# Optimization experiments

Hardware: AMD Instinct MI355X
Metric: run time of the kernel (lower is better)

The kernel has to match this reference:

```python
import jax, jax.numpy as jnp
import numpy as np

N_ENT, E, M, STEPS, B, H, C = 500000, 128, 8, 3, 4096, 256, 16

def setup_inputs() -> dict:
    key = jax.random.key(0)
    ks = jax.random.split(key, 13)
    s = 0.05
    return {
        "entity_ids": jax.random.randint(ks[0], (B, STEPS + 1), 0, N_ENT),
        "module_ids": jax.random.randint(ks[1], (B, STEPS), 0, M),
        "embedding": jax.random.normal(ks[2], (N_ENT, E), jnp.float32),
        "W_in": jax.random.normal(ks[3], (M, E, E), jnp.float32) * s,
        "b_in": jax.random.normal(ks[4], (M, E), jnp.float32) * s,
        "W_bias": jax.random.normal(ks[5], (M, E, E), jnp.float32) * s,
        "b_bias": jax.random.normal(ks[6], (M, E), jnp.float32) * s,
        "W_f": jax.random.normal(ks[7], (M, 2 * E, E), jnp.float32) * s,
        "b_f": jax.random.normal(ks[8], (M, E), jnp.float32) * s,
        "W1": jax.random.normal(ks[9], (E, H), jnp.float32) * s,
        "b1": jax.random.normal(ks[10], (H,), jnp.float32) * s,
        "W2": jax.random.normal(ks[11], (H, C), jnp.float32) * s,
        "b2": jax.random.normal(ks[12], (C,), jnp.float32) * s,
    }

def reference(entity_ids, module_ids, embedding, W_in, b_in, W_bias, b_bias,
              W_f, b_f, W1, b1, W2, b2):
    # x: [B, E] embedding of each path's start entity
    x = embedding[entity_ids[:, 0]]

    def step(x, inputs):
        mid, eid = inputs                      # [B], [B]
        bias = embedding[eid]                  # [B, E]
        h_in = jax.nn.relu(jnp.einsum('be,beo->bo', x, W_in[mid]) + b_in[mid])
        h_bi = jax.nn.relu(jnp.einsum('be,beo->bo', bias, W_bias[mid]) + b_bias[mid])
        h = jnp.concatenate([h_in, h_bi], axis=1)  # [B, 2E]
        x_new = jnp.tanh(jnp.einsum('bf,bfo->bo', h, W_f[mid]) + b_f[mid])
        return x_new, None

    xs = (module_ids.T, entity_ids[:, 1:].T)   # [STEPS, B] each
    x, _ = jax.lax.scan(step, x, xs)

    # classifier: Linear -> ReLU -> Linear
    h = jax.nn.relu(x @ W1 + b1)
    return h @ W2 + b2
```

## Files before the change

### kernel.cpp

```cpp
#include <hip/hip_runtime.h>

#define BB      4096
#define EE      128
#define MM      8
#define NSTEPS  3
#define HH      256
#define CC      16

#define TS      16
#define FB      1024

#define NFRAGBLK 1096

#define NSEG    8
#define GRIDN   256
#define PREP_GRID (NFRAGBLK + NSTEPS*NSEG + 8)

typedef __attribute__((ext_vector_type(8))) short  bf16x8;
typedef __attribute__((ext_vector_type(4))) float  f32x4;

__device__ __forceinline__ unsigned short bf16_rn(float v) {
    unsigned u = __float_as_uint(v);
    return (unsigned short)((u + 0x7FFFu + ((u >> 16) & 1u)) >> 16);
}
__device__ __forceinline__ float bf16_f(unsigned short h) {
    return __uint_as_float(((unsigned)h) << 16);
}
__device__ __forceinline__ void split8(const float* v, bf16x8& hi, bf16x8& lo) {
    #pragma unroll
    for (int i = 0; i < 8; i++) {
        unsigned short h = bf16_rn(v[i]);
        hi[i] = (short)h;
        lo[i] = (short)bf16_rn(v[i] - bf16_f(h));
    }
}
__device__ __forceinline__ void split1(float v, unsigned short& h, unsigned short& l) {
    h = bf16_rn(v);
    l = bf16_rn(v - bf16_f(h));
}
#define MFMA(a,b,c) __builtin_amdgcn_mfma_f32_16x16x32_bf16((a),(b),(c),0,0,0)
__device__ __forceinline__ f32x4 mfma3(bf16x8 ah, bf16x8 al, bf16x8 bh, bf16x8 bl, f32x4 c) {
    c = MFMA(ah, bh, c);
    c = MFMA(ah, bl, c);
    c = MFMA(al, bh, c);
    return c;
}

__global__ __launch_bounds__(512) void prep_kernel(
    const int*   __restrict__ module_ids,
    const float* __restrict__ W_in, const float* __restrict__ W_bias,
    const float* __restrict__ W_f,  const float* __restrict__ W1,
    const float* __restrict__ W2,
    unsigned short* __restrict__ wf,
    int* __restrict__ wcnt, int* __restrict__ perm, int* __restrict__ fl)
{
    const int vb = blockIdx.x, tid = threadIdx.x;
    __shared__ int wc8[8][MM];

    if (vb < NFRAGBLK) {
        unsigned short* dhi = wf + (size_t)vb * FB;
        unsigned short* dlo = dhi + 512;
        const int el = tid;
        const int ln = el >> 3, j = el & 7;
        const int krel = ((ln >> 4) << 3) + j;
        const int nrel = ln & 15;
        float v;
        if (vb < 512) {
            const int bb = vb & 255;
            const int kc = bb & 3, nt = (bb >> 2) & 7, m = bb >> 5;
            const float* src = (vb < 256 ? W_in : W_bias) + (size_t)m * EE * EE;
            v = src[(size_t)(kc*32 + krel) * EE + nt*16 + nrel];
        } else if (vb < 1024) {
            const int bb = vb - 512;
            const int kc = bb & 7, nt = (bb >> 3) & 7, m = bb >> 6;
            v = W_f[(size_t)m * 2*EE*EE + (size_t)(kc*32 + krel) * EE + nt*16 + nrel];
        } else if (vb < 1088) {
            const int bb = vb - 1024;
            const int kc = bb & 3, nt = bb >> 2;
            v = W1[(size_t)(kc*32 + krel) * HH + nt*16 + nrel];
        } else {
            const int kc = vb - 1088;
            v = W2[(size_t)(kc*32 + krel) * CC + nrel];
        }
        split1(v, dhi[el], dlo[el]);
    } else if (vb < NFRAGBLK + NSTEPS*NSEG) {
        const int u = vb - NFRAGBLK;
        const int t = u >> 3, seg = u & 7;
        const int lane = tid & 63, wave = tid >> 6;
        const int s = seg*512 + tid;
        const int m = module_ids[s*NSTEPS + t];
        unsigned long long mybal = 0ull, lanebal = 0ull;
        #pragma unroll
        for (int k = 0; k < MM; k++) {
            const unsigned long long bk = __ballot(m == k);
            if (m == k)    mybal   = bk;
            if (lane == k) lanebal = bk;
        }
        if (lane < MM) wc8[wave][lane] = __popcll(lanebal);
        __syncthreads();
        int base = 0;
        #pragma unroll
        for (int w = 0; w < 8; w++) if (w < wave) base += wc8[w][m];
        const unsigned long long below = (1ull << lane) - 1ull;
        const int rank = __popcll(mybal & below);
        perm[(((t*MM + m)*NSEG) + seg)*512 + base + rank] = s;
        if (tid < MM) {
            int sum = 0;
            #pragma unroll
            for (int w = 0; w < 8; w++) sum += wc8[w][tid];
            wcnt[((t*MM + tid)*NSEG) + seg] = sum;
        }
    } else {
        const int u = vb - NFRAGBLK - NSTEPS*NSEG;
        fl[u*512 + tid] = 0;
    }
}

__global__ __launch_bounds__(512, 2) void steps_kernel(
    const int*   __restrict__ entity_ids,
    const float* __restrict__ embedding,
    const float* __restrict__ b_in, const float* __restrict__ b_bias,
    const float* __restrict__ b_f,
    const float* __restrict__ b1v, const float* __restrict__ b2,
    const unsigned short* __restrict__ wf,
    const int* __restrict__ wcnt, const int* __restrict__ perm,
    unsigned short* __restrict__ xsh, unsigned short* __restrict__ xsl,
    int* __restrict__ fl, float* __restrict__ out)
{
    const int bx = blockIdx.x, tid = threadIdx.x;
    const int lane = tid & 63, wave = tid >> 6;
    const int row16 = lane & 15, quad = lane >> 4;

    __shared__ __align__(16) unsigned short hfh[8][512];
    __shared__ __align__(16) unsigned short hfl[8][512];
    __shared__ int   sids[TS];
    __shared__ float red[8][TS][CC];

    for (int t = 0; t < NSTEPS; t++) {
        int tot[MM];
        #pragma unroll
        for (int k = 0; k < MM; k++) {
            int s = 0;
            #pragma unroll
            for (int j = 0; j < NSEG; j++) s += wcnt[(t*MM + k)*NSEG + j];
            tot[k] = s;
        }
        int NB = 0;
        #pragma unroll
        for (int k = 0; k < MM; k++) NB += (tot[k] + TS - 1) >> 4;

        for (int pass = 0; pass < 2; pass++) {
            const int vb = bx + pass*GRIDN;
            if (vb >= NB) break;

            int m = -1, pref = 0, cm = 0, acc = 0;
            #pragma unroll
            for (int k = 0; k < MM; k++) {
                const int nbk = (tot[k] + TS - 1) >> 4;
                if (m < 0 && vb < acc + nbk) { m = k; pref = acc; cm = tot[k]; }
                acc += nbk;
            }
            const int chunk = vb - pref;

            __syncthreads();
            if (tid < TS) {
                const int sl = chunk*TS + tid;
                int sv = -1;
                if (sl < cm) {
                    int j = 0, r = sl;
                    while (true) {
                        const int c = wcnt[(t*MM + m)*NSEG + j];
                        if (r < c) break;
                        r -= c; j++;
                    }
                    sv = perm[((t*MM + m)*NSEG + j)*512 + r];
                }
                sids[tid] = sv;
            }
            __syncthreads();

            const int sA  = sids[row16];
            const int sAc = sA < 0 ? 0 : sA;

            bf16x8 xh[4], xl[4], eh[4], el_[4];
            const int eidb = entity_ids[sAc*(NSTEPS+1) + t + 1];
            const float* srcb = embedding + (size_t)eidb*EE;

            if (t == 0) {
                const int eid0 = entity_ids[sAc*(NSTEPS+1)];
                const float* src0 = embedding + (size_t)eid0*EE;
                #pragma unroll
                for (int kc = 0; kc < 4; kc++) {
                    const int off = kc*32 + quad*8;
                    float vv[8], bb[8];
                    *(float4*)(vv)     = *(const float4*)(src0 + off);
                    *(float4*)(vv + 4) = *(const float4*)(src0 + off + 4);
                    *(float4*)(bb)     = *(const float4*)(srcb + off);
                    *(float4*)(bb + 4) = *(const float4*)(srcb + off + 4);
                    split8(vv, xh[kc], xl[kc]);
                    split8(bb, eh[kc], el_[kc]);
                }
            } else {
                float bb[4][8];
                #pragma unroll
                for (int kc = 0; kc < 4; kc++) {
                    const int off = kc*32 + quad*8;
                    *(float4*)(bb[kc])     = *(const float4*)(srcb + off);
                    *(float4*)(bb[kc] + 4) = *(const float4*)(srcb + off + 4);
                }
                if (tid < TS && sids[tid] >= 0) {
                    int* f = &fl[sids[tid]];
                    while (__hip_atomic_load(f, __ATOMIC_RELAXED, __HIP_MEMORY_SCOPE_AGENT) < t)
                        __builtin_amdgcn_s_sleep(2);
                    (void)__hip_atomic_load(f, __ATOMIC_ACQUIRE, __HIP_MEMORY_SCOPE_AGENT);
                }
                __syncthreads();

                const unsigned short* xhp = xsh + (size_t)sAc*EE;
                const unsigned short* xlp = xsl + (size_t)sAc*EE;
                #pragma unroll
                for (int kc = 0; kc < 4; kc++) {
                    const int off = kc*32 + quad*8;
                    xh[kc] = *(const bf16x8*)(xhp + off);
                    xl[kc] = *(const bf16x8*)(xlp + off);
                    split8(bb[kc], eh[kc], el_[kc]);
                }
            }

            f32x4 aci = {0.f,0.f,0.f,0.f}, acb = {0.f,0.f,0.f,0.f};
            #pragma unroll
            for (int kc = 0; kc < 4; kc++) {
                const unsigned short* bI  = wf + (size_t)((m*8 + wave)*4 + kc)*FB;
                const unsigned short* bBp = wf + (size_t)(256 + (m*8 + wave)*4 + kc)*FB;
                const bf16x8 wih = *(const bf16x8*)(bI + lane*8);
                const bf16x8 wil = *(const bf16x8*)(bI + 512 + lane*8);
                const bf16x8 wbh = *(const bf16x8*)(bBp + lane*8);
                const bf16x8 wbl = *(const bf16x8*)(bBp + 512 + lane*8);
                aci = mfma3(xh[kc], xl[kc], wih, wil, aci);
                acb = mfma3(eh[kc], el_[kc], wbh, wbl, acb);
            }

            {
                const int col = wave*16 + row16;
                const float bin = b_in [m*EE + col];
                const float bbi = b_bias[m*EE + col];
                #pragma unroll
                for (int r = 0; r < 4; r++) {
                    const int row = quad*4 + r;
                    {
                        const float v = fmaxf(aci[r] + bin, 0.f);
                        const int k = col, kc = k >> 5;
                        const int idx = (row + 16*((k >> 3) & 3))*8 + (k & 7);
                        split1(v, hfh[kc][idx], hfl[kc][idx]);
                    }
                    {
                        const float v = fmaxf(acb[r] + bbi, 0.f);
                        const int k = EE + col, kc = k >> 5;
                        const int idx = (row + 16*((k >> 3) & 3))*8 + (k & 7);
                        split1(v, hfh[kc][idx], hfl[kc][idx]);
                    }
                }
            }
            __syncthreads();

            f32x4 acf = {0.f,0.f,0.f,0.f};
            #pragma unroll
            for (int kc = 0; kc < 8; kc++) {
                const bf16x8 ah = *(const bf16x8*)(&hfh[kc][lane*8]);
                const bf16x8 al = *(const bf16x8*)(&hfl[kc][lane*8]);
                const unsigned short* bF = wf + (size_t)(512 + (m*8 + wave)*8 + kc)*FB;
                const bf16x8 wfh = *(const bf16x8*)(bF + lane*8);
                const bf16x8 wfl = *(const bf16x8*)(bF + 512 + lane*8);
                acf = mfma3(ah, al, wfh, wfl, acf);
            }

            const int col = wave*16 + row16;
            const float bfv = b_f[m*EE + col];
            float xv[4];
            #pragma unroll
            for (int r = 0; r < 4; r++) xv[r] = tanhf(acf[r] + bfv);

            if (t < NSTEPS-1) {
                #pragma unroll
                for (int r = 0; r < 4; r++) {
                    const int s = sids[quad*4 + r];
                    if (s >= 0) {
                        unsigned short h, l;
                        split1(xv[r], h, l);
                        xsh[(size_t)s*EE + col] = h;
                        xsl[(size_t)s*EE + col] = l;
                    }
                }
                __syncthreads();
                if (tid < TS && sids[tid] >= 0)
                    __hip_atomic_store(&fl[sids[tid]], t+1,
                                       __ATOMIC_RELEASE, __HIP_MEMORY_SCOPE_AGENT);
            } else {
                __syncthreads();
                #pragma unroll
                for (int r = 0; r < 4; r++) {
                    const int row = quad*4 + r;
                    const int k = col, kc = k >> 5;
                    const int idx = (row + 16*((k >> 3) & 3))*8 + (k & 7);
                    split1(xv[r], hfh[kc][idx], hfl[kc][idx]);
                }
                __syncthreads();

                f32x4 a1[2] = {{0.f,0.f,0.f,0.f},{0.f,0.f,0.f,0.f}};
                #pragma unroll
                for (int i = 0; i < 2; i++) {
                    const int nt = wave + 8*i;
                    #pragma unroll
                    for (int kc = 0; kc < 4; kc++) {
                        const unsigned short* bW = wf + (size_t)(1024 + nt*4 + kc)*FB;
                        const bf16x8 wh = *(const bf16x8*)(bW + lane*8);
                        const bf16x8 wl = *(const bf16x8*)(bW + 512 + lane*8);
                        const bf16x8 ah = *(const bf16x8*)(&hfh[kc][lane*8]);
                        const bf16x8 al = *(const bf16x8*)(&hfl[kc][lane*8]);
                        a1[i] = mfma3(ah, al, wh, wl, a1[i]);
                    }
                }
                __syncthreads();
                #pragma unroll
                for (int i = 0; i < 2; i++) {
                    const int c2 = (wave + 8*i)*16 + row16;
                    const float b = b1v[c2];
                    #pragma unroll
                    for (int r = 0; r < 4; r++) {
                        const int row = quad*4 + r;
                        const float v = fmaxf(a1[i][r] + b, 0.f);
                        const int kc = c2 >> 5;
                        const int idx = (row + 16*((c2 >> 3) & 3))*8 + (c2 & 7);
                        split1(v, hfh[kc][idx], hfl[kc][idx]);
                    }
                }
                __syncthreads();

                f32x4 a2 = {0.f,0.f,0.f,0.f};
                {
                    const int kc = wave;
                    const bf16x8 ah = *(const bf16x8*)(&hfh[kc][lane*8]);
                    const bf16x8 al = *(const bf16x8*)(&hfl[kc][lane*8]);
                    const unsigned short* bW = wf + (size_t)(1088 + kc)*FB;
                    const bf16x8 wh = *(const bf16x8*)(bW + lane*8);
                    const bf16x8 wl = *(const bf16x8*)(bW + 512 + lane*8);
                    a2 = mfma3(ah, al, wh, wl, a2);
                }
                #pragma unroll
                for (int r = 0; r < 4; r++) red[wave][quad*4 + r][row16] = a2[r];
                __syncthreads();

                if (tid < TS*CC) {
                    const int sr = sids[tid >> 4];
                    if (sr >= 0) {
                        const int c = tid & 15;
                        float v = b2[c];
                        #pragma unroll
                        for (int w = 0; w < 8; w++) v += red[w][tid >> 4][c];
                        out[(size_t)sr*CC + c] = v;
                    }
                }
            }
        }
    }
}

extern "C" void kernel_launch(void* const* d_in, const int* in_sizes, int n_in,
                              void* d_out, int out_size, void* d_ws, size_t ws_size,
                              hipStream_t stream) {
    const int*   entity_ids = (const int*)  d_in[0];
    const int*   module_ids = (const int*)  d_in[1];
    const float* embedding  = (const float*)d_in[2];
    const float* W_in   = (const float*)d_in[3];
    const float* b_in   = (const float*)d_in[4];
    const float* W_bias = (const float*)d_in[5];
    const float* b_bias = (const float*)d_in[6];
    const float* W_f    = (const float*)d_in[7];
    const float* b_f    = (const float*)d_in[8];
    const float* W1     = (const float*)d_in[9];
    const float* b1     = (const float*)d_in[10];
    const float* W2     = (const float*)d_in[11];
    const float* b2     = (const float*)d_in[12];
    float* out = (float*)d_out;

    char* ws = (char*)d_ws;
    int* wcnt = (int*)(ws + 0);
    int* perm = (int*)(ws + 4096);
    int* fl   = (int*)(ws + (512u<<10));
    unsigned short* wfb = (unsigned short*)(ws + (1u<<20));
    unsigned short* xsh = (unsigned short*)(ws + (4u<<20));
    unsigned short* xsl = (unsigned short*)(ws + (5u<<20));

    prep_kernel<<<PREP_GRID, 512, 0, stream>>>(module_ids,
                                               W_in, W_bias, W_f, W1, W2,
                                               wfb, wcnt, perm, fl);

    void* sargs[] = { &entity_ids, &embedding, &b_in, &b_bias, &b_f,
                      &b1, &b2, &wfb, &wcnt, &perm, &xsh, &xsl, &fl, &out };
    hipError_t e = hipLaunchCooperativeKernel(
        reinterpret_cast<const void*>(steps_kernel),
        dim3(GRIDN), dim3(512), sargs, 0u, stream);
    if (e != hipSuccess) {
        (void)hipGetLastError();
        steps_kernel<<<GRIDN, 512, 0, stream>>>(entity_ids, embedding,
                                                b_in, b_bias, b_f, b1, b2,
                                                wfb, wcnt, perm, xsh, xsl, fl, out);
    }
}
```

Before: 406.4 us.

## Replace persistent cooperative kernel with per-step launches, dropping flag spin-waits

Replaces the single persistent cooperative steps kernel, which used per-sample flags and spin-waiting across steps, with one launch per step and a grid sized to the maximum number of 16-row chunks. Kernel boundaries now order the steps, so the flag array, its zeroing in prep, and the atomic acquire/release are removed. This trades the intra-kernel dependency polling for two extra launches and full grid barriers between steps, and loses the chance for early chunks to overlap with the next step.

```diff
diff --git a/kernel.cpp b/kernel.cpp
--- a/kernel.cpp
+++ b/kernel.cpp
@@ -13,8 +13,8 @@
 #define NFRAGBLK 1096
 
 #define NSEG    8
-#define GRIDN   256
-#define PREP_GRID (NFRAGBLK + NSTEPS*NSEG + 8)
+#define NBMAX   (BB/TS + MM)
+#define PREP_GRID (NFRAGBLK + NSTEPS*NSEG)
 
 typedef __attribute__((ext_vector_type(8))) short  bf16x8;
 typedef __attribute__((ext_vector_type(4))) float  f32x4;
@@ -52,7 +52,7 @@
     const float* __restrict__ W_f,  const float* __restrict__ W1,
     const float* __restrict__ W2,
     unsigned short* __restrict__ wf,
-    int* __restrict__ wcnt, int* __restrict__ perm, int* __restrict__ fl)
+    int* __restrict__ wcnt, int* __restrict__ perm)
 {
     const int vb = blockIdx.x, tid = threadIdx.x;
     __shared__ int wc8[8][MM];
@@ -83,7 +83,7 @@
             v = W2[(size_t)(kc*32 + krel) * CC + nrel];
         }
         split1(v, dhi[el], dlo[el]);
-    } else if (vb < NFRAGBLK + NSTEPS*NSEG) {
+    } else {
         const int u = vb - NFRAGBLK;
         const int t = u >> 3, seg = u & 7;
         const int lane = tid & 63, wave = tid >> 6;
@@ -110,13 +110,11 @@
             for (int w = 0; w < 8; w++) sum += wc8[w][tid];
             wcnt[((t*MM + tid)*NSEG) + seg] = sum;
         }
-    } else {
-        const int u = vb - NFRAGBLK - NSTEPS*NSEG;
-        fl[u*512 + tid] = 0;
-    }
-}
-
-__global__ __launch_bounds__(512, 2) void steps_kernel(
+    }
+}
+
+__global__ __launch_bounds__(512, 2) void step_kernel(
+    const int t,
     const int*   __restrict__ entity_ids,
     const float* __restrict__ embedding,
     const float* __restrict__ b_in, const float* __restrict__ b_bias,
@@ -125,241 +123,214 @@
     const unsigned short* __restrict__ wf,
     const int* __restrict__ wcnt, const int* __restrict__ perm,
     unsigned short* __restrict__ xsh, unsigned short* __restrict__ xsl,
-    int* __restrict__ fl, float* __restrict__ out)
+    float* __restrict__ out)
 {
     const int bx = blockIdx.x, tid = threadIdx.x;
     const int lane = tid & 63, wave = tid >> 6;
     const int row16 = lane & 15, quad = lane >> 4;
 
+    int tot[MM];
+    #pragma unroll
+    for (int k = 0; k < MM; k++) {
+        int s = 0;
+        #pragma unroll
+        for (int j = 0; j < NSEG; j++) s += wcnt[(t*MM + k)*NSEG + j];
+        tot[k] = s;
+    }
+    int m = -1, pref = 0, cm = 0, acc = 0;
+    #pragma unroll
+    for (int k = 0; k < MM; k++) {
+        const int nbk = (tot[k] + TS - 1) >> 4;
+        if (m < 0 && bx < acc + nbk) { m = k; pref = acc; cm = tot[k]; }
+        acc += nbk;
+    }
+    if (m < 0) return;
+    const int chunk = bx - pref;
+
     __shared__ __align__(16) unsigned short hfh[8][512];
     __shared__ __align__(16) unsigned short hfl[8][512];
     __shared__ int   sids[TS];
     __shared__ float red[8][TS][CC];
 
-    for (int t = 0; t < NSTEPS; t++) {
-        int tot[MM];
-        #pragma unroll
-        for (int k = 0; k < MM; k++) {
-            int s = 0;
-            #pragma unroll
-            for (int j = 0; j < NSEG; j++) s += wcnt[(t*MM + k)*NSEG + j];
-            tot[k] = s;
-        }
-        int NB = 0;
-        #pragma unroll
-        for (int k = 0; k < MM; k++) NB += (tot[k] + TS - 1) >> 4;
-
-        for (int pass = 0; pass < 2; pass++) {
-            const int vb = bx + pass*GRIDN;
-            if (vb >= NB) break;
-
-            int m = -1, pref = 0, cm = 0, acc = 0;
-            #pragma unroll
-            for (int k = 0; k < MM; k++) {
-                const int nbk = (tot[k] + TS - 1) >> 4;
-                if (m < 0 && vb < acc + nbk) { m = k; pref = acc; cm = tot[k]; }
-                acc += nbk;
-            }
-            const int chunk = vb - pref;
-
-            __syncthreads();
-            if (tid < TS) {
-                const int sl = chunk*TS + tid;
-                int sv = -1;
-                if (sl < cm) {
-                    int j = 0, r = sl;
-                    while (true) {
-                        const int c = wcnt[(t*MM + m)*NSEG + j];
-                        if (r < c) break;
-                        r -= c; j++;
-                    }
-                    sv = perm[((t*MM + m)*NSEG + j)*512 + r];
-                }
-                sids[tid] = sv;
-            }
-            __syncthreads();
-
-            const int sA  = sids[row16];
-            const int sAc = sA < 0 ? 0 : sA;
-
-            bf16x8 xh[4], xl[4], eh[4], el_[4];
-            const int eidb = entity_ids[sAc*(NSTEPS+1) + t + 1];
-            const float* srcb = embedding + (size_t)eidb*EE;
-
-            if (t == 0) {
-                const int eid0 = entity_ids[sAc*(NSTEPS+1)];
-                const float* src0 = embedding + (size_t)eid0*EE;
-                #pragma unroll
-                for (int kc = 0; kc < 4; kc++) {
-                    const int off = kc*32 + quad*8;
-                    float vv[8], bb[8];
-                    *(float4*)(vv)     = *(const float4*)(src0 + off);
-                    *(float4*)(vv + 4) = *(const float4*)(src0 + off + 4);
-                    *(float4*)(bb)     = *(const float4*)(srcb + off);
-                    *(float4*)(bb + 4) = *(const float4*)(srcb + off + 4);
-                    split8(vv, xh[kc], xl[kc]);
-                    split8(bb, eh[kc], el_[kc]);
-                }
-            } else {
-                float bb[4][8];
-                #pragma unroll
-                for (int kc = 0; kc < 4; kc++) {
-                    const int off = kc*32 + quad*8;
-                    *(float4*)(bb[kc])     = *(const float4*)(srcb + off);
-                    *(float4*)(bb[kc] + 4) = *(const float4*)(srcb + off + 4);
-                }
-                if (tid < TS && sids[tid] >= 0) {
-                    int* f = &fl[sids[tid]];
-                    while (__hip_atomic_load(f, __ATOMIC_RELAXED, __HIP_MEMORY_SCOPE_AGENT) < t)
-                        __builtin_amdgcn_s_sleep(2);
-                    (void)__hip_atomic_load(f, __ATOMIC_ACQUIRE, __HIP_MEMORY_SCOPE_AGENT);
-                }
-                __syncthreads();
-
-                const unsigned short* xhp = xsh + (size_t)sAc*EE;
-                const unsigned short* xlp = xsl + (size_t)sAc*EE;
-                #pragma unroll
-                for (int kc = 0; kc < 4; kc++) {
-                    const int off = kc*32 + quad*8;
-                    xh[kc] = *(const bf16x8*)(xhp + off);
-                    xl[kc] = *(const bf16x8*)(xlp + off);
-                    split8(bb[kc], eh[kc], el_[kc]);
-                }
-            }
-
-            f32x4 aci = {0.f,0.f,0.f,0.f}, acb = {0.f,0.f,0.f,0.f};
+    if (tid < TS) {
+        const int sl = chunk*TS + tid;
+        int sv = -1;
+        if (sl < cm) {
+            int j = 0, r = sl;
+            while (true) {
+                const int c = wcnt[(t*MM + m)*NSEG + j];
+                if (r < c) break;
+                r -= c; j++;
+            }
+            sv = perm[((t*MM + m)*NSEG + j)*512 + r];
+        }
+        sids[tid] = sv;
+    }
+    __syncthreads();
+
+    const int sA  = sids[row16];
+    const int sAc = sA < 0 ? 0 : sA;
+
+    bf16x8 xh[4], xl[4], eh[4], el_[4];
+    const int eidb = entity_ids[sAc*(NSTEPS+1) + t + 1];
+    const float* srcb = embedding + (size_t)eidb*EE;
+
+    if (t == 0) {
+        const int eid0 = entity_ids[sAc*(NSTEPS+1)];
+        const float* src0 = embedding + (size_t)eid0*EE;
+        #pragma unroll
+        for (int kc = 0; kc < 4; kc++) {
+            const int off = kc*32 + quad*8;
+            float vv[8], bb[8];
+            *(float4*)(vv)     = *(const float4*)(src0 + off);
+            *(float4*)(vv + 4) = *(const float4*)(src0 + off + 4);
+            *(float4*)(bb)     = *(const float4*)(srcb + off);
+            *(float4*)(bb + 4) = *(const float4*)(srcb + off + 4);
+            split8(vv, xh[kc], xl[kc]);
+            split8(bb, eh[kc], el_[kc]);
+        }
+    } else {
+        const unsigned short* xhp = xsh + (size_t)sAc*EE;
+        const unsigned short* xlp = xsl + (size_t)sAc*EE;
+        #pragma unroll
+        for (int kc = 0; kc < 4; kc++) {
+            const int off = kc*32 + quad*8;
+            float bb[8];
+            *(float4*)(bb)     = *(const float4*)(srcb + off);
+            *(float4*)(bb + 4) = *(const float4*)(srcb + off + 4);
+            xh[kc] = *(const bf16x8*)(xhp + off);
+            xl[kc] = *(const bf16x8*)(xlp + off);
+            split8(bb, eh[kc], el_[kc]);
+        }
+    }
+
+    f32x4 aci = {0.f,0.f,0.f,0.f}, acb = {0.f,0.f,0.f,0.f};
+    #pragma unroll
+    for (int kc = 0; kc < 4; kc++) {
+        const unsigned short* bI  = wf + (size_t)((m*8 + wave)*4 + kc)*FB;
+        const unsigned short* bBp = wf + (size_t)(256 + (m*8 + wave)*4 + kc)*FB;
+        const bf16x8 wih = *(const bf16x8*)(bI + lane*8);
+        const bf16x8 wil = *(const bf16x8*)(bI + 512 + lane*8);
+        const bf16x8 wbh = *(const bf16x8*)(bBp + lane*8);
+        const bf16x8 wbl = *(const bf16x8*)(bBp + 512 + lane*8);
+        aci = mfma3(xh[kc], xl[kc], wih, wil, aci);
+        acb = mfma3(eh[kc], el_[kc], wbh, wbl, acb);
+    }
+
+    {
+        const int col = wave*16 + row16;
+        const float bin = b_in [m*EE + col];
+        const float bbi = b_bias[m*EE + col];
+        #pragma unroll
+        for (int r = 0; r < 4; r++) {
+            const int row = quad*4 + r;
+            {
+                const float v = fmaxf(aci[r] + bin, 0.f);
+                const int k = col, kc = k >> 5;
+                const int idx = (row + 16*((k >> 3) & 3))*8 + (k & 7);
+                split1(v, hfh[kc][idx], hfl[kc][idx]);
+            }
+            {
+                const float v = fmaxf(acb[r] + bbi, 0.f);
+                const int k = EE + col, kc = k >> 5;
+                const int idx = (row + 16*((k >> 3) & 3))*8 + (k & 7);
+                split1(v, hfh[kc][idx], hfl[kc][idx]);
+            }
+        }
+    }
+    __syncthreads();
+
+    f32x4 acf = {0.f,0.f,0.f,0.f};
+    #pragma unroll
+    for (int kc = 0; kc < 8; kc++) {
+        const bf16x8 ah = *(const bf16x8*)(&hfh[kc][lane*8]);
+        const bf16x8 al = *(const bf16x8*)(&hfl[kc][lane*8]);
+        const unsigned short* bF = wf + (size_t)(512 + (m*8 + wave)*8 + kc)*FB;
+        const bf16x8 wfh = *(const bf16x8*)(bF + lane*8);
+        const bf16x8 wfl = *(const bf16x8*)(bF + 512 + lane*8);
+        acf = mfma3(ah, al, wfh, wfl, acf);
+    }
+
+    const int col = wave*16 + row16;
+    const float bfv = b_f[m*EE + col];
+    float xv[4];
+    #pragma unroll
+    for (int r = 0; r < 4; r++) xv[r] = tanhf(acf[r] + bfv);
+
+    if (t < NSTEPS-1) {
+        #pragma unroll
+        for (int r = 0; r < 4; r++) {
+            const int s = sids[quad*4 + r];
+            if (s >= 0) {
+                unsigned short h, l;
+                split1(xv[r], h, l);
+                xsh[(size_t)s*EE + col] = h;
+                xsl[(size_t)s*EE + col] = l;
+            }
+        }
+    } else {
+        __syncthreads();
+        #pragma unroll
+        for (int r = 0; r < 4; r++) {
+            const int row = quad*4 + r;
+            const int k = col, kc = k >> 5;
+            const int idx = (row + 16*((k >> 3) & 3))*8 + (k & 7);
+            split1(xv[r], hfh[kc][idx], hfl[kc][idx]);
+        }
+        __syncthreads();
+
+        f32x4 a1[2] = {{0.f,0.f,0.f,0.f},{0.f,0.f,0.f,0.f}};
+        #pragma unroll
+        for (int i = 0; i < 2; i++) {
+            const int nt = wave + 8*i;
             #pragma unroll
             for (int kc = 0; kc < 4; kc++) {
-                const unsigned short* bI  = wf + (size_t)((m*8 + wave)*4 + kc)*FB;
-                const unsigned short* bBp = wf + (size_t)(256 + (m*8 + wave)*4 + kc)*FB;
-                const bf16x8 wih = *(const bf16x8*)(bI + lane*8);
-                const bf16x8 wil = *(const bf16x8*)(bI + 512 + lane*8);
-                const bf16x8 wbh = *(const bf16x8*)(bBp + lane*8);
-                const bf16x8 wbl = *(const bf16x8*)(bBp + 512 + lane*8);
-                aci = mfma3(xh[kc], xl[kc], wih, wil, aci);
-                acb = mfma3(eh[kc], el_[kc], wbh, wbl, acb);
-            }
-
-            {
-                const int col = wave*16 + row16;
-                const float bin = b_in [m*EE + col];
-                const float bbi = b_bias[m*EE + col];
-                #pragma unroll
-                for (int r = 0; r < 4; r++) {
-                    const int row = quad*4 + r;
-                    {
-                        const float v = fmaxf(aci[r] + bin, 0.f);
-                        const int k = col, kc = k >> 5;
-                        const int idx = (row + 16*((k >> 3) & 3))*8 + (k & 7);
-                        split1(v, hfh[kc][idx], hfl[kc][idx]);
-                    }
-                    {
-                        const float v = fmaxf(acb[r] + bbi, 0.f);
-                        const int k = EE + col, kc = k >> 5;
-                        const int idx = (row + 16*((k >> 3) & 3))*8 + (k & 7);
-                        split1(v, hfh[kc][idx], hfl[kc][idx]);
-                    }
-                }
-            }
-            __syncthreads();
-
-            f32x4 acf = {0.f,0.f,0.f,0.f};
-            #pragma unroll
-            for (int kc = 0; kc < 8; kc++) {
+                const unsigned short* bW = wf + (size_t)(1024 + nt*4 + kc)*FB;
+                const bf16x8 wh = *(const bf16x8*)(bW + lane*8);
+                const bf16x8 wl = *(const bf16x8*)(bW + 512 + lane*8);
                 const bf16x8 ah = *(const bf16x8*)(&hfh[kc][lane*8]);
                 const bf16x8 al = *(const bf16x8*)(&hfl[kc][lane*8]);
-                const unsigned short* bF = wf + (size_t)(512 + (m*8 + wave)*8 + kc)*FB;
-                const bf16x8 wfh = *(const bf16x8*)(bF + lane*8);
-                const bf16x8 wfl = *(const bf16x8*)(bF + 512 + lane*8);
-                acf = mfma3(ah, al, wfh, wfl, acf);
-            }
-
-            const int col = wave*16 + row16;
-            const float bfv = b_f[m*EE + col];
-            float xv[4];
+                a1[i] = mfma3(ah, al, wh, wl, a1[i]);
+            }
+        }
+        __syncthreads();
+        #pragma unroll
+        for (int i = 0; i < 2; i++) {
+            const int c2 = (wave + 8*i)*16 + row16;
+            const float b = b1v[c2];
             #pragma unroll
-            for (int r = 0; r < 4; r++) xv[r] = tanhf(acf[r] + bfv);
-
-            if (t < NSTEPS-1) {
+            for (int r = 0; r < 4; r++) {
+                const int row = quad*4 + r;
+                const float v = fmaxf(a1[i][r] + b, 0.f);
+                const int kc = c2 >> 5;
+                const int idx = (row + 16*((c2 >> 3) & 3))*8 + (c2 & 7);
+                split1(v, hfh[kc][idx], hfl[kc][idx]);
+            }
+        }
+        __syncthreads();
+
+        f32x4 a2 = {0.f,0.f,0.f,0.f};
+        {
+            const int kc = wave;
+            const bf16x8 ah = *(const bf16x8*)(&hfh[kc][lane*8]);
+            const bf16x8 al = *(const bf16x8*)(&hfl[kc][lane*8]);
+            const unsigned short* bW = wf + (size_t)(1088 + kc)*FB;
+            const bf16x8 wh = *(const bf16x8*)(bW + lane*8);
+            const bf16x8 wl = *(const bf16x8*)(bW + 512 + lane*8);
+            a2 = mfma3(ah, al, wh, wl, a2);
+        }
+        #pragma unroll
+        for (int r = 0; r < 4; r++) red[wave][quad*4 + r][row16] = a2[r];
+        __syncthreads();
+
+        if (tid < TS*CC) {
+            const int sr = sids[tid >> 4];
+            if (sr >= 0) {
+                const int c = tid & 15;
+                float v = b2[c];
                 #pragma unroll
-                for (int r = 0; r < 4; r++) {
-                    const int s = sids[quad*4 + r];
-                    if (s >= 0) {
-                        unsigned short h, l;
-                        split1(xv[r], h, l);
-                        xsh[(size_t)s*EE + col] = h;
-                        xsl[(size_t)s*EE + col] = l;
-                    }
-                }
-                __syncthreads();
-                if (tid < TS && sids[tid] >= 0)
-                    __hip_atomic_store(&fl[sids[tid]], t+1,
-                                       __ATOMIC_RELEASE, __HIP_MEMORY_SCOPE_AGENT);
-            } else {
-                __syncthreads();
-                #pragma unroll
-                for (int r = 0; r < 4; r++) {
-                    const int row = quad*4 + r;
-                    const int k = col, kc = k >> 5;
-                    const int idx = (row + 16*((k >> 3) & 3))*8 + (k & 7);
-                    split1(xv[r], hfh[kc][idx], hfl[kc][idx]);
-                }
-                __syncthreads();
-
-                f32x4 a1[2] = {{0.f,0.f,0.f,0.f},{0.f,0.f,0.f,0.f}};
-                #pragma unroll
-                for (int i = 0; i < 2; i++) {
-                    const int nt = wave + 8*i;
-                    #pragma unroll
-                    for (int kc = 0; kc < 4; kc++) {
-                        const unsigned short* bW = wf + (size_t)(1024 + nt*4 + kc)*FB;
-                        const bf16x8 wh = *(const bf16x8*)(bW + lane*8);
-                        const bf16x8 wl = *(const bf16x8*)(bW + 512 + lane*8);
-                        const bf16x8 ah = *(const bf16x8*)(&hfh[kc][lane*8]);
-                        const bf16x8 al = *(const bf16x8*)(&hfl[kc][lane*8]);
-                        a1[i] = mfma3(ah, al, wh, wl, a1[i]);
-                    }
-                }
-                __syncthreads();
-                #pragma unroll
-                for (int i = 0; i < 2; i++) {
-                    const int c2 = (wave + 8*i)*16 + row16;
-                    const float b = b1v[c2];
-                    #pragma unroll
-                    for (int r = 0; r < 4; r++) {
-                        const int row = quad*4 + r;
-                        const float v = fmaxf(a1[i][r] + b, 0.f);
-                        const int kc = c2 >> 5;
-                        const int idx = (row + 16*((c2 >> 3) & 3))*8 + (c2 & 7);
-                        split1(v, hfh[kc][idx], hfl[kc][idx]);
-                    }
-                }
-                __syncthreads();
-
-                f32x4 a2 = {0.f,0.f,0.f,0.f};
-                {
-                    const int kc = wave;
-                    const bf16x8 ah = *(const bf16x8*)(&hfh[kc][lane*8]);
-                    const bf16x8 al = *(const bf16x8*)(&hfl[kc][lane*8]);
-                    const unsigned short* bW = wf + (size_t)(1088 + kc)*FB;
-                    const bf16x8 wh = *(const bf16x8*)(bW + lane*8);
-                    const bf16x8 wl = *(const bf16x8*)(bW + 512 + lane*8);
-                    a2 = mfma3(ah, al, wh, wl, a2);
-                }
-                #pragma unroll
-                for (int r = 0; r < 4; r++) red[wave][quad*4 + r][row16] = a2[r];
-                __syncthreads();
-
-                if (tid < TS*CC) {
-                    const int sr = sids[tid >> 4];
-                    if (sr >= 0) {
-                        const int c = tid & 15;
-                        float v = b2[c];
-                        #pragma unroll
-                        for (int w = 0; w < 8; w++) v += red[w][tid >> 4][c];
-                        out[(size_t)sr*CC + c] = v;
-                    }
-                }
+                for (int w = 0; w < 8; w++) v += red[w][tid >> 4][c];
+                out[(size_t)sr*CC + c] = v;
             }
         }
     }
@@ -386,24 +357,16 @@
     char* ws = (char*)d_ws;
     int* wcnt = (int*)(ws + 0);
     int* perm = (int*)(ws + 4096);
-    int* fl   = (int*)(ws + (512u<<10));
     unsigned short* wfb = (unsigned short*)(ws + (1u<<20));
     unsigned short* xsh = (unsigned short*)(ws + (4u<<20));
     unsigned short* xsl = (unsigned short*)(ws + (5u<<20));
 
     prep_kernel<<<PREP_GRID, 512, 0, stream>>>(module_ids,
                                                W_in, W_bias, W_f, W1, W2,
-                                               wfb, wcnt, perm, fl);
-
-    void* sargs[] = { &entity_ids, &embedding, &b_in, &b_bias, &b_f,
-                      &b1, &b2, &wfb, &wcnt, &perm, &xsh, &xsl, &fl, &out };
-    hipError_t e = hipLaunchCooperativeKernel(
-        reinterpret_cast<const void*>(steps_kernel),
-        dim3(GRIDN), dim3(512), sargs, 0u, stream);
-    if (e != hipSuccess) {
-        (void)hipGetLastError();
-        steps_kernel<<<GRIDN, 512, 0, stream>>>(entity_ids, embedding,
-                                                b_in, b_bias, b_f, b1, b2,
-                                                wfb, wcnt, perm, xsh, xsl, fl, out);
-    }
-}
+                                               wfb, wcnt, perm);
+    for (int t = 0; t < NSTEPS; t++) {
+        step_kernel<<<NBMAX, 512, 0, stream>>>(t, entity_ids, embedding,
+                                               b_in, b_bias, b_f, b1, b2,
+                                               wfb, wcnt, perm, xsh, xsl, out);
+    }
+}
```

Measured after the change: 365.7 us. 10.0% less time.
